# Performance work log

Measured on AMD Instinct MI355X. Metric: run time of the kernel, lower is better.

Reference implementation:

```python
import jax, jax.numpy as jnp
import numpy as np

WS = 7            # window size
NW = 64           # windows per image ((56/7)^2)
SHIFT = 3         # shift size for the SW-MSA mask
HW = 56           # spatial patch grid


def _build_rel_index():
    coords = np.stack(np.meshgrid(np.arange(WS), np.arange(WS), indexing='ij'))  # [2,7,7]
    flat = coords.reshape(2, -1)                                                 # [2,49]
    rel = (flat[:, :, None] - flat[:, None, :]).transpose(1, 2, 0)               # [49,49,2]
    rel[:, :, 0] += WS - 1
    rel[:, :, 1] += WS - 1
    rel[:, :, 0] *= 2 * WS - 1
    return rel.sum(-1).astype(np.int32)                                          # [49,49]


def _build_shift_mask():
    img = np.zeros((HW, HW), dtype=np.float32)
    cnt = 0
    sl = (slice(0, -WS), slice(-WS, -SHIFT), slice(-SHIFT, None))
    for h in sl:
        for w in sl:
            img[h, w] = cnt
            cnt += 1
    # window partition -> [nW, 49]
    mw = img.reshape(HW // WS, WS, HW // WS, WS).transpose(0, 2, 1, 3).reshape(-1, WS * WS)
    am = mw[:, None, :] - mw[:, :, None]                                          # [nW,49,49]
    return np.where(am != 0, -100.0, 0.0).astype(np.float32)


def setup_inputs() -> dict:
    key = jax.random.key(0)
    ks = jax.random.split(key, 6)
    dim, heads, N = 128, 4, WS * WS
    B_ = 4096
    return {
        'x': jax.random.normal(ks[0], (B_, N, dim), dtype=jnp.float32),
        'qkv_w': jax.random.normal(ks[1], (dim, 3 * dim), dtype=jnp.float32) * 0.02,
        'qkv_b': jax.random.normal(ks[2], (3 * dim,), dtype=jnp.float32) * 0.02,
        'proj_w': jax.random.normal(ks[3], (dim, dim), dtype=jnp.float32) * 0.02,
        'proj_b': jax.random.normal(ks[4], (dim,), dtype=jnp.float32) * 0.02,
        'rel_bias_table': jax.random.normal(ks[5], ((2 * WS - 1) ** 2, heads), dtype=jnp.float32) * 0.02,
        'mask': jnp.asarray(_build_shift_mask()),
        'rel_index': jnp.asarray(_build_rel_index()),
    }


def reference(x, qkv_w, qkv_b, proj_w, proj_b, rel_bias_table, mask, rel_index):
    B_, N, C = x.shape
    heads = rel_bias_table.shape[1]
    hd = C // heads
    scale = hd ** -0.5
    # fused qkv projection: [B_, N, 3, H, hd]
    qkv = (x @ qkv_w + qkv_b).reshape(B_, N, 3, heads, hd)
    q, k, v = qkv[:, :, 0], qkv[:, :, 1], qkv[:, :, 2]      # [B_, N, H, hd]
    attn = jnp.einsum('bnhd,bmhd->bhnm', q, k) * scale       # [B_, H, N, N]
    # relative position bias gather: [N,N,H] -> [H,N,N]
    bias = rel_bias_table[rel_index].transpose(2, 0, 1)
    attn = attn + bias[None]
    # shifted-window mask: mask [nW, N, N]
    nW = mask.shape[0]
    attn = attn.reshape(B_ // nW, nW, heads, N, N) + mask[None, :, None]
    attn = attn.reshape(B_, heads, N, N)
    attn = jax.nn.softmax(attn, axis=-1)
    out = jnp.einsum('bhnm,bmhd->bnhd', attn, v).reshape(B_, N, C)
    return out @ proj_w + proj_b
```

## Files before the change

kernel.cpp:

```cpp
#include <hip/hip_runtime.h>
#include <hip/hip_bf16.h>

typedef __attribute__((ext_vector_type(8))) short bf16x8;
typedef __attribute__((ext_vector_type(4))) short s16x4;
typedef __attribute__((ext_vector_type(4))) float f32x4;

#define NTOK 49

__device__ __forceinline__ short f2b(float v) {
    __hip_bfloat16 b = __float2bfloat16(v);
    return *reinterpret_cast<short*>(&b);
}

__device__ __forceinline__ int rid_of(int t, int wh, int ww) {
    int i = t / 7;
    int j = t - 7 * i;
    int rh = (wh == 7) ? ((i < 4) ? 1 : 2) : 0;
    int rw = (ww == 7) ? ((j < 4) ? 1 : 2) : 0;
    return rh * 3 + rw;
}

__global__ void prep_kernel(const float* __restrict__ qkv_w,
                            const float* __restrict__ proj_w,
                            const float* __restrict__ rel_tab,
                            const int*   __restrict__ rel_idx,
                            short* __restrict__ wqkv_t,
                            short* __restrict__ wproj_t,
                            float* __restrict__ bmp) {
    int i = blockIdx.x * 256 + threadIdx.x;
    if (i < 384 * 128) {
        int n = i >> 7, k = i & 127;
        wqkv_t[i] = f2b(qkv_w[k * 384 + n]);
        return;
    }
    int j = i - 384 * 128;
    if (j < 128 * 128) {
        int n = j >> 7, k = j & 127;
        wproj_t[j] = f2b(proj_w[k * 128 + n]);
        return;
    }
    int l = j - 128 * 128;
    if (l < 4 * NTOK * 64) {
        int h = l / (NTOK * 64);
        int rem = l - h * (NTOK * 64);
        int q = rem >> 6, kk = rem & 63;
        bmp[l] = (kk < NTOK) ? rel_tab[rel_idx[q * NTOK + kk] * 4 + h] : 0.0f;
    }
}

#define XB_BASE   0
#define XB_STR    136
#define HREG_BASE 6664
#define HREG_SZ   3920
#define QB_STR    40
#define PB_STR    72
#define VBT_BASE  22344
#define VBT_SZ    2304
#define VBT_STR   72

__launch_bounds__(512, 4)
__global__ void swin_fused(const float* __restrict__ x,
                           const short* __restrict__ wqkv_t,
                           const float* __restrict__ qkv_b,
                           const short* __restrict__ wproj_t,
                           const float* __restrict__ proj_b,
                           const float* __restrict__ bmp,
                           float* __restrict__ out) {
    __shared__ short sm[31560];

    const int b   = blockIdx.x;
    const int tid = threadIdx.x;
    const int wv  = tid >> 6;
    const int ln  = tid & 63;
    const int g   = ln >> 4;
    const int c   = ln & 15;
    const int h    = wv >> 1;
    const int half = wv & 1;

    short* qbh  = sm + HREG_BASE + h * HREG_SZ;
    short* kbh  = qbh + NTOK * QB_STR;
    short* pbh  = qbh;
    short* vbt  = sm + VBT_BASE + h * VBT_SZ;

    {
        const f32x4* xp4 = (const f32x4*)(x + (size_t)b * (NTOK * 128));
        for (int idx = tid; idx < NTOK * 32; idx += 512) {
            f32x4 v = xp4[idx];
            int e0 = idx * 4;
            int row = e0 >> 7, col = e0 & 127;
            s16x4 pk;
            pk[0] = f2b(v[0]); pk[1] = f2b(v[1]); pk[2] = f2b(v[2]); pk[3] = f2b(v[3]);
            *(s16x4*)&sm[XB_BASE + row * XB_STR + col] = pk;
        }
    }
    __syncthreads();

    {
        const int bases[3] = { 32*h + 16*half, 128 + 32*h + 16*half, 256 + 32*h + 16*half };
        f32x4 acc[3][4];
        #pragma unroll
        for (int t = 0; t < 3; ++t)
            #pragma unroll
            for (int nt = 0; nt < 4; ++nt) acc[t][nt] = (f32x4){0.f,0.f,0.f,0.f};
        #pragma unroll
        for (int kt = 0; kt < 4; ++kt) {
            bf16x8 aw[3];
            #pragma unroll
            for (int t = 0; t < 3; ++t)
                aw[t] = *(const bf16x8*)&wqkv_t[(bases[t] + c) * 128 + 32*kt + 8*g];
            bf16x8 xv[4];
            #pragma unroll
            for (int nt = 0; nt < 4; ++nt) {
                int tok = 16*nt + c; if (tok > 48) tok = 48;
                xv[nt] = *(const bf16x8*)&sm[XB_BASE + tok * XB_STR + 32*kt + 8*g];
            }
            #pragma unroll
            for (int t = 0; t < 3; ++t)
                #pragma unroll
                for (int nt = 0; nt < 4; ++nt)
                    acc[t][nt] = __builtin_amdgcn_mfma_f32_16x16x32_bf16(aw[t], xv[nt], acc[t][nt], 0, 0, 0);
        }
        const float scale = 0.17677669529663687f;
        #pragma unroll
        for (int t = 0; t < 3; ++t) {
            f32x4 b4 = *(const f32x4*)&qkv_b[bases[t] + 4*g];
            #pragma unroll
            for (int nt = 0; nt < 4; ++nt) {
                int tok = 16*nt + c;
                if (tok >= NTOK) continue;
                float v0 = acc[t][nt][0] + b4[0];
                float v1 = acc[t][nt][1] + b4[1];
                float v2 = acc[t][nt][2] + b4[2];
                float v3 = acc[t][nt][3] + b4[3];
                if (t == 0) { v0 *= scale; v1 *= scale; v2 *= scale; v3 *= scale; }
                if (t < 2) {
                    s16x4 pk; pk[0]=f2b(v0); pk[1]=f2b(v1); pk[2]=f2b(v2); pk[3]=f2b(v3);
                    short* dst = (t == 0) ? qbh : kbh;
                    *(s16x4*)&dst[tok * QB_STR + 16*half + 4*g] = pk;
                } else {
                    int d0 = 16*half + 4*g;
                    vbt[(d0+0) * VBT_STR + tok] = f2b(v0);
                    vbt[(d0+1) * VBT_STR + tok] = f2b(v1);
                    vbt[(d0+2) * VBT_STR + tok] = f2b(v2);
                    vbt[(d0+3) * VBT_STR + tok] = f2b(v3);
                }
            }
        }
        for (int i2 = ln; i2 < 16 * 15; i2 += 64) {
            int d = 16*half + i2 / 15;
            int t = 49 + i2 % 15;
            vbt[d * VBT_STR + t] = 0;
        }
    }
    __syncthreads();

    const int ntq0 = 2 * half;
    f32x4 sA[4][2];
    {
        #pragma unroll
        for (int mt = 0; mt < 4; ++mt) { sA[mt][0] = (f32x4){0.f,0.f,0.f,0.f}; sA[mt][1] = (f32x4){0.f,0.f,0.f,0.f}; }
        bf16x8 ak[4];
        #pragma unroll
        for (int mt = 0; mt < 4; ++mt) {
            int kt2 = 16*mt + c; if (kt2 > 48) kt2 = 48;
            ak[mt] = *(const bf16x8*)&kbh[kt2 * QB_STR + 8*g];
        }
        #pragma unroll
        for (int jj = 0; jj < 2; ++jj) {
            int qt = 16*(ntq0+jj) + c; if (qt > 48) qt = 48;
            bf16x8 bq = *(const bf16x8*)&qbh[qt * QB_STR + 8*g];
            #pragma unroll
            for (int mt = 0; mt < 4; ++mt)
                sA[mt][jj] = __builtin_amdgcn_mfma_f32_16x16x32_bf16(ak[mt], bq, sA[mt][jj], 0, 0, 0);
        }
    }
    __syncthreads();

    {
        const int wh = (b >> 3) & 7, ww = b & 7;
        const bool wmask = (wh == 7) || (ww == 7);
        int ridk[16];
        if (wmask) {
            #pragma unroll
            for (int mt = 0; mt < 4; ++mt)
                #pragma unroll
                for (int r = 0; r < 4; ++r) {
                    int ktok = 16*mt + 4*g + r;
                    ridk[4*mt+r] = rid_of(ktok < NTOK ? ktok : 48, wh, ww);
                }
        }
        #pragma unroll
        for (int jj = 0; jj < 2; ++jj) {
            int qtok = 16*(ntq0+jj) + c;
            int qtokc = qtok > 48 ? 48 : qtok;
            int ridq = wmask ? rid_of(qtokc, wh, ww) : 0;
            const float* bp = bmp + ((size_t)h * NTOK + qtokc) * 64;
            float e[16];
            float mx = -1e30f;
            #pragma unroll
            for (int mt = 0; mt < 4; ++mt) {
                f32x4 b4 = *(const f32x4*)&bp[16*mt + 4*g];
                #pragma unroll
                for (int r = 0; r < 4; ++r) {
                    int ktok = 16*mt + 4*g + r;
                    float v = sA[mt][jj][r] + b4[r];
                    bool ok = (ktok < NTOK) && (!wmask || (ridk[4*mt+r] == ridq));
                    v = ok ? v : -1e30f;
                    e[4*mt+r] = v;
                    mx = fmaxf(mx, v);
                }
            }
            mx = fmaxf(mx, __shfl_xor(mx, 16, 64));
            mx = fmaxf(mx, __shfl_xor(mx, 32, 64));
            float s = 0.f;
            #pragma unroll
            for (int ii = 0; ii < 16; ++ii) { float ev = __expf(e[ii] - mx); e[ii] = ev; s += ev; }
            s += __shfl_xor(s, 16, 64);
            s += __shfl_xor(s, 32, 64);
            float rs = 1.0f / s;
            if (qtok < NTOK) {
                #pragma unroll
                for (int mt = 0; mt < 4; ++mt) {
                    s16x4 pk;
                    pk[0] = f2b(e[4*mt+0] * rs);
                    pk[1] = f2b(e[4*mt+1] * rs);
                    pk[2] = f2b(e[4*mt+2] * rs);
                    pk[3] = f2b(e[4*mt+3] * rs);
                    *(s16x4*)&pbh[qtok * PB_STR + 16*mt + 4*g] = pk;
                }
            }
        }
    }

    {
        f32x4 o[2][2];
        o[0][0]=(f32x4){0.f,0.f,0.f,0.f}; o[0][1]=(f32x4){0.f,0.f,0.f,0.f};
        o[1][0]=(f32x4){0.f,0.f,0.f,0.f}; o[1][1]=(f32x4){0.f,0.f,0.f,0.f};
        #pragma unroll
        for (int kt = 0; kt < 2; ++kt) {
            bf16x8 av[2];
            #pragma unroll
            for (int mt = 0; mt < 2; ++mt)
                av[mt] = *(const bf16x8*)&vbt[(16*mt + c) * VBT_STR + 32*kt + 8*g];
            #pragma unroll
            for (int jj = 0; jj < 2; ++jj) {
                int qt = 16*(ntq0+jj) + c; if (qt > 48) qt = 48;
                bf16x8 bp2 = *(const bf16x8*)&pbh[qt * PB_STR + 32*kt + 8*g];
                #pragma unroll
                for (int mt = 0; mt < 2; ++mt)
                    o[mt][jj] = __builtin_amdgcn_mfma_f32_16x16x32_bf16(av[mt], bp2, o[mt][jj], 0, 0, 0);
            }
        }
        #pragma unroll
        for (int jj = 0; jj < 2; ++jj) {
            int qtok = 16*(ntq0+jj) + c;
            if (qtok >= NTOK) continue;
            #pragma unroll
            for (int mt = 0; mt < 2; ++mt) {
                s16x4 pk;
                pk[0] = f2b(o[mt][jj][0]); pk[1] = f2b(o[mt][jj][1]);
                pk[2] = f2b(o[mt][jj][2]); pk[3] = f2b(o[mt][jj][3]);
                *(s16x4*)&sm[XB_BASE + qtok * XB_STR + 32*h + 16*mt + 4*g] = pk;
            }
        }
    }
    __syncthreads();

    {
        const int chb = 16 * wv;
        f32x4 po[4];
        #pragma unroll
        for (int j = 0; j < 4; ++j) po[j] = (f32x4){0.f,0.f,0.f,0.f};
        #pragma unroll
        for (int kt = 0; kt < 4; ++kt) {
            bf16x8 aw = *(const bf16x8*)&wproj_t[(chb + c) * 128 + 32*kt + 8*g];
            #pragma unroll
            for (int j = 0; j < 4; ++j) {
                int qt = 16*j + c; if (qt > 48) qt = 48;
                bf16x8 bo = *(const bf16x8*)&sm[XB_BASE + qt * XB_STR + 32*kt + 8*g];
                po[j] = __builtin_amdgcn_mfma_f32_16x16x32_bf16(aw, bo, po[j], 0, 0, 0);
            }
        }
        f32x4 pb4 = *(const f32x4*)&proj_b[chb + 4*g];
        float* op = out + (size_t)b * (NTOK * 128);
        #pragma unroll
        for (int j = 0; j < 4; ++j) {
            int qtok = 16*j + c;
            if (qtok >= NTOK) continue;
            f32x4 w;
            w[0] = po[j][0] + pb4[0]; w[1] = po[j][1] + pb4[1];
            w[2] = po[j][2] + pb4[2]; w[3] = po[j][3] + pb4[3];
            *(f32x4*)&op[qtok * 128 + chb + 4*g] = w;
        }
    }
}

extern "C" void kernel_launch(void* const* d_in, const int* in_sizes, int n_in,
                              void* d_out, int out_size, void* d_ws, size_t ws_size,
                              hipStream_t stream) {
    const float* x       = (const float*)d_in[0];
    const float* qkv_w   = (const float*)d_in[1];
    const float* qkv_b   = (const float*)d_in[2];
    const float* proj_w  = (const float*)d_in[3];
    const float* proj_b  = (const float*)d_in[4];
    const float* rel_tab = (const float*)d_in[5];
    const int*   rel_idx = (const int*)d_in[7];

    char* ws = (char*)d_ws;
    short* wqkv_t  = (short*)ws;
    short* wproj_t = (short*)(ws + 98304);
    float* bmp     = (float*)(ws + 98304 + 32768);

    int total = 384*128 + 128*128 + 4*NTOK*64;
    prep_kernel<<<(total + 255) / 256, 256, 0, stream>>>(qkv_w, proj_w, rel_tab, rel_idx,
                                                         wqkv_t, wproj_t, bmp);

    int B_ = in_sizes[0] / (NTOK * 128);
    swin_fused<<<B_, 512, 0, stream>>>(x, wqkv_t, qkv_b, wproj_t, proj_b, bmp,
                                       (float*)d_out);
}
```

Measured before the change: 129.0 us.

## Shrink shared memory via buffer aliasing and register-resident softmax probabilities

Overlaps the V-transpose buffer with the x tile, splitting the QKV projection into a Q/K pass and a V pass separated by a barrier, so shared memory drops and launch bounds rise to six blocks per CU. Softmax probabilities now stay in registers and are redistributed with cross-lane shuffles into the MFMA B operand instead of going through an LDS P buffer. This removes one barrier, and bias and V loads are issued before the QK^T MFMAs. The price is extra shuffles, tighter register limits that may cause spills, and an extra sync in the projection phase.

```diff
diff --git a/kernel.cpp b/kernel.cpp
--- a/kernel.cpp
+++ b/kernel.cpp
@@ -10,6 +10,19 @@
 __device__ __forceinline__ short f2b(float v) {
     __hip_bfloat16 b = __float2bfloat16(v);
     return *reinterpret_cast<short*>(&b);
+}
+
+__device__ __forceinline__ s16x4 shfl64(s16x4 v, int src) {
+    long long x = *reinterpret_cast<long long*>(&v);
+    x = __shfl(x, src, 64);
+    return *reinterpret_cast<s16x4*>(&x);
+}
+
+__device__ __forceinline__ bf16x8 cat8(s16x4 lo, s16x4 hi) {
+    bf16x8 r;
+    r[0]=lo[0]; r[1]=lo[1]; r[2]=lo[2]; r[3]=lo[3];
+    r[4]=hi[0]; r[5]=hi[1]; r[6]=hi[2]; r[7]=hi[3];
+    return r;
 }
 
 __device__ __forceinline__ int rid_of(int t, int wh, int ww) {
@@ -48,17 +61,7 @@
     }
 }
 
-#define XB_BASE   0
-#define XB_STR    136
-#define HREG_BASE 6664
-#define HREG_SZ   3920
-#define QB_STR    40
-#define PB_STR    72
-#define VBT_BASE  22344
-#define VBT_SZ    2304
-#define VBT_STR   72
-
-__launch_bounds__(512, 4)
+__launch_bounds__(512, 6)
 __global__ void swin_fused(const float* __restrict__ x,
                            const short* __restrict__ wqkv_t,
                            const float* __restrict__ qkv_b,
@@ -66,7 +69,7 @@
                            const float* __restrict__ proj_b,
                            const float* __restrict__ bmp,
                            float* __restrict__ out) {
-    __shared__ short sm[31560];
+    __shared__ short sm[24896];
 
     const int b   = blockIdx.x;
     const int tid = threadIdx.x;
@@ -77,106 +80,142 @@
     const int h    = wv >> 1;
     const int half = wv & 1;
 
-    short* qbh  = sm + HREG_BASE + h * HREG_SZ;
-    short* kbh  = qbh + NTOK * QB_STR;
-    short* pbh  = qbh;
-    short* vbt  = sm + VBT_BASE + h * VBT_SZ;
-
-    {
-        const f32x4* xp4 = (const f32x4*)(x + (size_t)b * (NTOK * 128));
-        for (int idx = tid; idx < NTOK * 32; idx += 512) {
-            f32x4 v = xp4[idx];
-            int e0 = idx * 4;
-            int row = e0 >> 7, col = e0 & 127;
-            s16x4 pk;
-            pk[0] = f2b(v[0]); pk[1] = f2b(v[1]); pk[2] = f2b(v[2]); pk[3] = f2b(v[3]);
-            *(s16x4*)&sm[XB_BASE + row * XB_STR + col] = pk;
-        }
+    short* qbh = sm + 9216 + h * 3920;
+    short* kbh = qbh + 1960;
+    short* vbt = sm + h * 2304;
+
+    {
+        const f32x4* xp4 = (const f32x4*)(x + (size_t)b * 6272);
+        f32x4 v0 = xp4[tid];
+        f32x4 v1 = xp4[tid + 512];
+        f32x4 v2 = xp4[tid + 1024];
+        f32x4 v3;
+        if (tid < 32) v3 = xp4[tid + 1536];
+        #define XWR(IDX, V) { int row = (IDX) >> 5; int col = ((IDX) & 31) * 4; \
+            s16x4 pk; pk[0]=f2b((V)[0]); pk[1]=f2b((V)[1]); pk[2]=f2b((V)[2]); pk[3]=f2b((V)[3]); \
+            *(s16x4*)&sm[row * 136 + col] = pk; }
+        XWR(tid, v0) XWR(tid + 512, v1) XWR(tid + 1024, v2)
+        if (tid < 32) XWR(tid + 1536, v3)
+        #undef XWR
     }
     __syncthreads();
 
-    {
-        const int bases[3] = { 32*h + 16*half, 128 + 32*h + 16*half, 256 + 32*h + 16*half };
-        f32x4 acc[3][4];
-        #pragma unroll
-        for (int t = 0; t < 3; ++t)
-            #pragma unroll
-            for (int nt = 0; nt < 4; ++nt) acc[t][nt] = (f32x4){0.f,0.f,0.f,0.f};
+    const int cq = 32 * h + 16 * half;
+
+    {
+        f32x4 accq[4], acck[4];
+        #pragma unroll
+        for (int nt = 0; nt < 4; ++nt) { accq[nt] = (f32x4){0.f,0.f,0.f,0.f}; acck[nt] = (f32x4){0.f,0.f,0.f,0.f}; }
         #pragma unroll
         for (int kt = 0; kt < 4; ++kt) {
-            bf16x8 aw[3];
-            #pragma unroll
-            for (int t = 0; t < 3; ++t)
-                aw[t] = *(const bf16x8*)&wqkv_t[(bases[t] + c) * 128 + 32*kt + 8*g];
+            bf16x8 awq = *(const bf16x8*)&wqkv_t[(cq + c) * 128 + 32*kt + 8*g];
+            bf16x8 awk = *(const bf16x8*)&wqkv_t[(128 + cq + c) * 128 + 32*kt + 8*g];
             bf16x8 xv[4];
             #pragma unroll
             for (int nt = 0; nt < 4; ++nt) {
                 int tok = 16*nt + c; if (tok > 48) tok = 48;
-                xv[nt] = *(const bf16x8*)&sm[XB_BASE + tok * XB_STR + 32*kt + 8*g];
-            }
-            #pragma unroll
-            for (int t = 0; t < 3; ++t)
-                #pragma unroll
-                for (int nt = 0; nt < 4; ++nt)
-                    acc[t][nt] = __builtin_amdgcn_mfma_f32_16x16x32_bf16(aw[t], xv[nt], acc[t][nt], 0, 0, 0);
-        }
-        const float scale = 0.17677669529663687f;
-        #pragma unroll
-        for (int t = 0; t < 3; ++t) {
-            f32x4 b4 = *(const f32x4*)&qkv_b[bases[t] + 4*g];
+                xv[nt] = *(const bf16x8*)&sm[tok * 136 + 32*kt + 8*g];
+            }
             #pragma unroll
             for (int nt = 0; nt < 4; ++nt) {
-                int tok = 16*nt + c;
-                if (tok >= NTOK) continue;
-                float v0 = acc[t][nt][0] + b4[0];
-                float v1 = acc[t][nt][1] + b4[1];
-                float v2 = acc[t][nt][2] + b4[2];
-                float v3 = acc[t][nt][3] + b4[3];
-                if (t == 0) { v0 *= scale; v1 *= scale; v2 *= scale; v3 *= scale; }
-                if (t < 2) {
-                    s16x4 pk; pk[0]=f2b(v0); pk[1]=f2b(v1); pk[2]=f2b(v2); pk[3]=f2b(v3);
-                    short* dst = (t == 0) ? qbh : kbh;
-                    *(s16x4*)&dst[tok * QB_STR + 16*half + 4*g] = pk;
-                } else {
-                    int d0 = 16*half + 4*g;
-                    vbt[(d0+0) * VBT_STR + tok] = f2b(v0);
-                    vbt[(d0+1) * VBT_STR + tok] = f2b(v1);
-                    vbt[(d0+2) * VBT_STR + tok] = f2b(v2);
-                    vbt[(d0+3) * VBT_STR + tok] = f2b(v3);
-                }
-            }
+                accq[nt] = __builtin_amdgcn_mfma_f32_16x16x32_bf16(awq, xv[nt], accq[nt], 0, 0, 0);
+                acck[nt] = __builtin_amdgcn_mfma_f32_16x16x32_bf16(awk, xv[nt], acck[nt], 0, 0, 0);
+            }
+        }
+        const float qsc = 0.17677669529663687f;
+        f32x4 bq4 = *(const f32x4*)&qkv_b[cq + 4*g];
+        f32x4 bk4 = *(const f32x4*)&qkv_b[128 + cq + 4*g];
+        #pragma unroll
+        for (int nt = 0; nt < 4; ++nt) {
+            int tok = 16*nt + c;
+            if (tok >= NTOK) continue;
+            s16x4 pq, pk2;
+            #pragma unroll
+            for (int r = 0; r < 4; ++r) {
+                pq[r]  = f2b((accq[nt][r] + bq4[r]) * qsc);
+                pk2[r] = f2b(acck[nt][r] + bk4[r]);
+            }
+            *(s16x4*)&qbh[tok * 40 + 16*half + 4*g] = pq;
+            *(s16x4*)&kbh[tok * 40 + 16*half + 4*g] = pk2;
+        }
+    }
+
+    {
+        f32x4 accv[4];
+        #pragma unroll
+        for (int nt = 0; nt < 4; ++nt) accv[nt] = (f32x4){0.f,0.f,0.f,0.f};
+        #pragma unroll
+        for (int kt = 0; kt < 4; ++kt) {
+            bf16x8 awv = *(const bf16x8*)&wqkv_t[(256 + cq + c) * 128 + 32*kt + 8*g];
+            bf16x8 xv[4];
+            #pragma unroll
+            for (int nt = 0; nt < 4; ++nt) {
+                int tok = 16*nt + c; if (tok > 48) tok = 48;
+                xv[nt] = *(const bf16x8*)&sm[tok * 136 + 32*kt + 8*g];
+            }
+            #pragma unroll
+            for (int nt = 0; nt < 4; ++nt)
+                accv[nt] = __builtin_amdgcn_mfma_f32_16x16x32_bf16(awv, xv[nt], accv[nt], 0, 0, 0);
+        }
+        __syncthreads();
+        f32x4 bv4 = *(const f32x4*)&qkv_b[256 + cq + 4*g];
+        const int d0 = 16*half + 4*g;
+        #pragma unroll
+        for (int nt = 0; nt < 4; ++nt) {
+            int tok = 16*nt + c;
+            if (tok >= NTOK) continue;
+            vbt[(d0+0) * 72 + tok] = f2b(accv[nt][0] + bv4[0]);
+            vbt[(d0+1) * 72 + tok] = f2b(accv[nt][1] + bv4[1]);
+            vbt[(d0+2) * 72 + tok] = f2b(accv[nt][2] + bv4[2]);
+            vbt[(d0+3) * 72 + tok] = f2b(accv[nt][3] + bv4[3]);
         }
         for (int i2 = ln; i2 < 16 * 15; i2 += 64) {
             int d = 16*half + i2 / 15;
             int t = 49 + i2 % 15;
-            vbt[d * VBT_STR + t] = 0;
+            vbt[d * 72 + t] = 0;
         }
     }
     __syncthreads();
 
     const int ntq0 = 2 * half;
-    f32x4 sA[4][2];
-    {
+    {
+        int qtok0 = 16*ntq0 + c;  int q0c = qtok0 > 48 ? 48 : qtok0;
+        const float* bp0 = bmp + ((size_t)h * NTOK + q0c) * 64;
+        f32x4 bias0[4];
+        #pragma unroll
+        for (int mt = 0; mt < 4; ++mt) bias0[mt] = *(const f32x4*)&bp0[16*mt + 4*g];
+
+        f32x4 sA[4][2];
         #pragma unroll
         for (int mt = 0; mt < 4; ++mt) { sA[mt][0] = (f32x4){0.f,0.f,0.f,0.f}; sA[mt][1] = (f32x4){0.f,0.f,0.f,0.f}; }
         bf16x8 ak[4];
         #pragma unroll
         for (int mt = 0; mt < 4; ++mt) {
             int kt2 = 16*mt + c; if (kt2 > 48) kt2 = 48;
-            ak[mt] = *(const bf16x8*)&kbh[kt2 * QB_STR + 8*g];
+            ak[mt] = *(const bf16x8*)&kbh[kt2 * 40 + 8*g];
         }
         #pragma unroll
         for (int jj = 0; jj < 2; ++jj) {
             int qt = 16*(ntq0+jj) + c; if (qt > 48) qt = 48;
-            bf16x8 bq = *(const bf16x8*)&qbh[qt * QB_STR + 8*g];
+            bf16x8 bq = *(const bf16x8*)&qbh[qt * 40 + 8*g];
             #pragma unroll
             for (int mt = 0; mt < 4; ++mt)
                 sA[mt][jj] = __builtin_amdgcn_mfma_f32_16x16x32_bf16(ak[mt], bq, sA[mt][jj], 0, 0, 0);
         }
-    }
-    __syncthreads();
-
-    {
+
+        int qtok1 = 16*(ntq0+1) + c;  int q1c = qtok1 > 48 ? 48 : qtok1;
+        const float* bp1 = bmp + ((size_t)h * NTOK + q1c) * 64;
+        f32x4 bias1[4];
+        #pragma unroll
+        for (int mt = 0; mt < 4; ++mt) bias1[mt] = *(const f32x4*)&bp1[16*mt + 4*g];
+
+        bf16x8 av[2][2];
+        #pragma unroll
+        for (int kt = 0; kt < 2; ++kt)
+            #pragma unroll
+            for (int mt = 0; mt < 2; ++mt)
+                av[kt][mt] = *(const bf16x8*)&vbt[(16*mt + c) * 72 + 32*kt + 8*g];
+
         const int wh = (b >> 3) & 7, ww = b & 7;
         const bool wmask = (wh == 7) || (ww == 7);
         int ridk[16];
@@ -189,21 +228,27 @@
                     ridk[4*mt+r] = rid_of(ktok < NTOK ? ktok : 48, wh, ww);
                 }
         }
+
+        f32x4 o[2][2];
+        o[0][0]=(f32x4){0.f,0.f,0.f,0.f}; o[0][1]=(f32x4){0.f,0.f,0.f,0.f};
+        o[1][0]=(f32x4){0.f,0.f,0.f,0.f}; o[1][1]=(f32x4){0.f,0.f,0.f,0.f};
+        const int srcL = 32*(g & 1) + c;
+        const int srcH = srcL + 16;
+
         #pragma unroll
         for (int jj = 0; jj < 2; ++jj) {
             int qtok = 16*(ntq0+jj) + c;
             int qtokc = qtok > 48 ? 48 : qtok;
             int ridq = wmask ? rid_of(qtokc, wh, ww) : 0;
-            const float* bp = bmp + ((size_t)h * NTOK + qtokc) * 64;
+            const f32x4* bias = jj ? bias1 : bias0;
             float e[16];
             float mx = -1e30f;
             #pragma unroll
             for (int mt = 0; mt < 4; ++mt) {
-                f32x4 b4 = *(const f32x4*)&bp[16*mt + 4*g];
                 #pragma unroll
                 for (int r = 0; r < 4; ++r) {
                     int ktok = 16*mt + 4*g + r;
-                    float v = sA[mt][jj][r] + b4[r];
+                    float v = sA[mt][jj][r] + bias[mt][r];
                     bool ok = (ktok < NTOK) && (!wmask || (ridk[4*mt+r] == ridq));
                     v = ok ? v : -1e30f;
                     e[4*mt+r] = v;
@@ -218,49 +263,35 @@
             s += __shfl_xor(s, 16, 64);
             s += __shfl_xor(s, 32, 64);
             float rs = 1.0f / s;
-            if (qtok < NTOK) {
-                #pragma unroll
-                for (int mt = 0; mt < 4; ++mt) {
-                    s16x4 pk;
-                    pk[0] = f2b(e[4*mt+0] * rs);
-                    pk[1] = f2b(e[4*mt+1] * rs);
-                    pk[2] = f2b(e[4*mt+2] * rs);
-                    pk[3] = f2b(e[4*mt+3] * rs);
-                    *(s16x4*)&pbh[qtok * PB_STR + 16*mt + 4*g] = pk;
-                }
-            }
-        }
-    }
-
-    {
-        f32x4 o[2][2];
-        o[0][0]=(f32x4){0.f,0.f,0.f,0.f}; o[0][1]=(f32x4){0.f,0.f,0.f,0.f};
-        o[1][0]=(f32x4){0.f,0.f,0.f,0.f}; o[1][1]=(f32x4){0.f,0.f,0.f,0.f};
-        #pragma unroll
-        for (int kt = 0; kt < 2; ++kt) {
-            bf16x8 av[2];
-            #pragma unroll
-            for (int mt = 0; mt < 2; ++mt)
-                av[mt] = *(const bf16x8*)&vbt[(16*mt + c) * VBT_STR + 32*kt + 8*g];
-            #pragma unroll
-            for (int jj = 0; jj < 2; ++jj) {
-                int qt = 16*(ntq0+jj) + c; if (qt > 48) qt = 48;
-                bf16x8 bp2 = *(const bf16x8*)&pbh[qt * PB_STR + 32*kt + 8*g];
+            s16x4 pk[4];
+            #pragma unroll
+            for (int m = 0; m < 4; ++m) {
+                pk[m][0] = f2b(e[4*m+0] * rs); pk[m][1] = f2b(e[4*m+1] * rs);
+                pk[m][2] = f2b(e[4*m+2] * rs); pk[m][3] = f2b(e[4*m+3] * rs);
+            }
+            #pragma unroll
+            for (int kt = 0; kt < 2; ++kt) {
+                s16x4 aL  = shfl64(pk[2*kt],     srcL);
+                s16x4 aLb = shfl64(pk[2*kt + 1], srcL);
+                s16x4 aH  = shfl64(pk[2*kt],     srcH);
+                s16x4 aHb = shfl64(pk[2*kt + 1], srcH);
+                bf16x8 B = cat8((g < 2) ? aL : aLb, (g < 2) ? aH : aHb);
                 #pragma unroll
                 for (int mt = 0; mt < 2; ++mt)
-                    o[mt][jj] = __builtin_amdgcn_mfma_f32_16x16x32_bf16(av[mt], bp2, o[mt][jj], 0, 0, 0);
-            }
-        }
+                    o[mt][jj] = __builtin_amdgcn_mfma_f32_16x16x32_bf16(av[kt][mt], B, o[mt][jj], 0, 0, 0);
+            }
+        }
+        __syncthreads();
         #pragma unroll
         for (int jj = 0; jj < 2; ++jj) {
             int qtok = 16*(ntq0+jj) + c;
             if (qtok >= NTOK) continue;
             #pragma unroll
             for (int mt = 0; mt < 2; ++mt) {
-                s16x4 pk;
-                pk[0] = f2b(o[mt][jj][0]); pk[1] = f2b(o[mt][jj][1]);
-                pk[2] = f2b(o[mt][jj][2]); pk[3] = f2b(o[mt][jj][3]);
-                *(s16x4*)&sm[XB_BASE + qtok * XB_STR + 32*h + 16*mt + 4*g] = pk;
+                s16x4 pko;
+                pko[0] = f2b(o[mt][jj][0]); pko[1] = f2b(o[mt][jj][1]);
+                pko[2] = f2b(o[mt][jj][2]); pko[3] = f2b(o[mt][jj][3]);
+                *(s16x4*)&sm[qtok * 136 + 32*h + 16*mt + 4*g] = pko;
             }
         }
     }
@@ -277,12 +308,12 @@
             #pragma unroll
             for (int j = 0; j < 4; ++j) {
                 int qt = 16*j + c; if (qt > 48) qt = 48;
-                bf16x8 bo = *(const bf16x8*)&sm[XB_BASE + qt * XB_STR + 32*kt + 8*g];
+                bf16x8 bo = *(const bf16x8*)&sm[qt * 136 + 32*kt + 8*g];
                 po[j] = __builtin_amdgcn_mfma_f32_16x16x32_bf16(aw, bo, po[j], 0, 0, 0);
             }
         }
         f32x4 pb4 = *(const f32x4*)&proj_b[chb + 4*g];
-        float* op = out + (size_t)b * (NTOK * 128);
+        float* op = out + (size_t)b * 6272;
         #pragma unroll
         for (int j = 0; j < 4; ++j) {
             int qtok = 16*j + c;
```

New measurement: 193.7 us. 50.1% more time.
